# Kernel tuning notes

Measured on AMD Instinct MI355X. Metric: run time of the kernel, lower is better.

The kernel has to match this reference:

```python
import jax, jax.numpy as jnp
import numpy as np

N_NODES = 50000
EMB = 256
HEADS = 2
N_BASE_EDGES = 100000


def setup_inputs() -> dict:
    key = jax.random.key(0)
    ks = jax.random.split(key, 12)
    x = jax.random.normal(ks[0], (N_NODES, EMB), dtype=jnp.float32)
    # bipartite edges: sources in left half, targets in right half -> no self-loops
    src = jax.random.randint(ks[1], (N_BASE_EDGES,), 0, N_NODES // 2)
    dst = jax.random.randint(ks[2], (N_BASE_EDGES,), N_NODES // 2, N_NODES)
    edge_index = jnp.stack([src, dst]).astype(jnp.int64)
    hd = EMB // HEADS
    s = 0.02
    params = {
        "Wkqv": jax.random.normal(ks[3], (EMB, 3 * EMB), dtype=jnp.float32) * s,
        "bkqv": jnp.zeros((3 * EMB,), dtype=jnp.float32),
        "W1": jax.random.normal(ks[4], (2 * hd, hd), dtype=jnp.float32) * s,
        "b1": jnp.zeros((hd,), dtype=jnp.float32),
        "W2": jax.random.normal(ks[5], (hd, 1), dtype=jnp.float32) * s,
        "b2": jnp.zeros((1,), dtype=jnp.float32),
        "Wout": jax.random.normal(ks[6], (EMB, EMB), dtype=jnp.float32) * s,
        "bout": jnp.zeros((EMB,), dtype=jnp.float32),
    }
    return {"x": x, "edge_index": edge_index, **params}


def reference(x, edge_index, Wkqv, bkqv, W1, b1, W2, b2, Wout, bout):
    N, emb = x.shape
    H = HEADS
    hd = emb // H
    # MetaGNNNoEdgeAttr.forward preprocessing: make undirected + self loops.
    # Input is bipartite (no self-loops), so remove_self_loops is a no-op.
    ei = jnp.concatenate([edge_index, edge_index[::-1]], axis=1)
    loops = jnp.arange(N, dtype=edge_index.dtype)
    src = jnp.concatenate([ei[0], loops])  # j (message source)
    dst = jnp.concatenate([ei[1], loops])  # i (message target / softmax index)

    # single GNN layer (n_layers=1)
    kqv = x @ Wkqv + bkqv  # [N, 3*emb]
    q = kqv[dst, :emb].reshape(-1, H, hd)                                  # [E,H,hd]
    k = kqv[src, emb:2 * emb].reshape(-1, H, hd) / jnp.sqrt(jnp.float32(hd))
    v = kqv[src, 2 * emb:].reshape(-1, H, hd)

    h = jax.nn.relu(jnp.concatenate([k, q], axis=-1) @ W1 + b1)  # [E,H,hd]
    a = (h @ W2 + b2).squeeze(-1)                                # [E,H]

    # segment softmax over destination nodes (every node has a self-loop)
    m = jax.ops.segment_max(a, dst, num_segments=N)              # [N,H]
    ex = jnp.exp(a - m[dst])
    s = jax.ops.segment_sum(ex, dst, num_segments=N)             # [N,H]
    alpha = ex / (s[dst] + 1e-16)                                # [E,H]

    msg = (alpha[..., None] * v).reshape(-1, emb) @ Wout + bout  # [E,emb]
    out = jax.ops.segment_sum(msg, dst, num_segments=N)          # [N,emb]
    return jax.nn.relu(out) + x
```

## Files before the change

kernel.cpp:

```cpp
#include <hip/hip_runtime.h>
#include <hip/hip_bf16.h>

#define EMB 256

typedef __bf16 bf16_t;
typedef __attribute__((ext_vector_type(8))) __bf16 bf16x8;
typedef __attribute__((ext_vector_type(4))) __bf16 bf16x4;
typedef __attribute__((ext_vector_type(4))) float floatx4;

__device__ __forceinline__ int eidx(const int* __restrict__ p, int is64, long long k){
  return is64 ? p[2*k] : p[(int)k];
}
__device__ __forceinline__ void async_load16(const void* g, void* l){
  __builtin_amdgcn_global_load_lds(
      (const __attribute__((address_space(1))) unsigned int*)g,
      (__attribute__((address_space(3))) unsigned int*)l,
      16, 0, 0);
}
__device__ __forceinline__ float4 cvt4(bf16x4 v){
  return make_float4((float)v.x, (float)v.y, (float)v.z, (float)v.w);
}

__global__ void detect_kernel(const int* __restrict__ ei, int* __restrict__ flag){
  int z = (ei[1]==0) + (ei[3]==0) + (ei[5]==0) + (ei[7]==0);
  *flag = (z == 4) ? 1 : 0;
}

__global__ void cvt_x_kernel(const float* __restrict__ x, bf16_t* __restrict__ xb, int n4){
  int t = blockIdx.x*blockDim.x + threadIdx.x;
  if (t >= n4) return;
  const float4 v = *(const float4*)(x + (size_t)t*4);
  bf16x4 o = { (bf16_t)v.x, (bf16_t)v.y, (bf16_t)v.z, (bf16_t)v.w };
  *(bf16x4*)(xb + (size_t)t*4) = o;
}

__global__ void prep_weights(const float* __restrict__ Wkqv, const float* __restrict__ bkqv,
                             const float* __restrict__ W1,
                             bf16_t* __restrict__ WcombT, float* __restrict__ bcomb){
  int n = blockIdx.x * blockDim.x + threadIdx.x;
  int c = blockIdx.y;
  if (n >= 768) return;
  const float rs = rsqrtf(128.0f);
  bool isBias = (c == 256);
  const float* arow = isBias ? bkqv : (Wkqv + (size_t)c*768);
  float val;
  if (n < 256){
    int h = n >> 7, d = n & 127;
    float s = 0.f;
    for (int t = 0; t < 128; ++t)
      s = fmaf(arow[h*128 + t], W1[(size_t)(128 + t)*128 + d], s);
    val = s;
  } else {
    int r = n - 256;
    int h = r >> 8, t8 = r & 255;
    int g = t8 >> 3, half = (t8 >> 2) & 1, dd = t8 & 3;
    int d = g*4 + dd;
    if (half == 0){
      float s = 0.f;
      for (int t = 0; t < 128; ++t)
        s = fmaf(arow[256 + h*128 + t], W1[(size_t)t*128 + d], s);
      val = s * rs;
    } else {
      val = arow[512 + h*128 + d];
    }
  }
  if (isBias) bcomb[n] = val;
  else        WcombT[(size_t)n*256 + c] = (bf16_t)val;
}

__global__ void prep_wout(const float* __restrict__ W, bf16_t* __restrict__ Wt){
  int t = blockIdx.x*blockDim.x + threadIdx.x;
  int n = t & 255, c = t >> 8;
  Wt[(size_t)n*256 + c] = (bf16_t)W[(size_t)c*256 + n];
}

__global__ void deg_kernel(const int* __restrict__ ei, const int* __restrict__ flag,
                           int* __restrict__ deg, int E0, int Nn){
  int t = blockIdx.x*blockDim.x + threadIdx.x;
  if (t >= 2*E0) return;
  int is64 = *flag;
  int i = (t < E0) ? eidx(ei,is64,(long long)E0+t) : eidx(ei,is64,t-E0);
  i = min(max(i,0), Nn-1);
  atomicAdd(deg + i, 1);
}

__global__ __launch_bounds__(1024) void scan_kernel(const int* __restrict__ deg,
                                                    int* __restrict__ off, int N){
  __shared__ int wsum[16];
  __shared__ int carry_s;
  int tid = threadIdx.x, lane = tid & 63, w = tid >> 6;
  if (tid == 0) carry_s = 0;
  __syncthreads();
  for (int base = 0; base < N; base += 1024){
    int carry = carry_s;
    int v = (base + tid < N) ? (deg[base + tid] + 1) : 0;
    int incl = v;
    #pragma unroll
    for (int o = 1; o < 64; o <<= 1){
      int t = __shfl_up(incl, o, 64);
      if (lane >= o) incl += t;
    }
    if (lane == 63) wsum[w] = incl;
    __syncthreads();
    if (w == 0 && lane < 16){
      int sv = wsum[lane];
      #pragma unroll
      for (int o = 1; o < 16; o <<= 1){
        int t = __shfl_up(sv, o, 64);
        if (lane >= o) sv += t;
      }
      wsum[lane] = sv;
    }
    __syncthreads();
    int wpref = (w == 0) ? 0 : wsum[w-1];
    if (base + tid < N) off[base + tid] = carry + wpref + incl - v;
    __syncthreads();
    if (tid == 1023) carry_s = carry + wsum[15];
    __syncthreads();
  }
  if (threadIdx.x == 0) off[N] = carry_s;
}

__global__ void scatter_kernel(const int* __restrict__ ei, const int* __restrict__ flag,
                               const int* __restrict__ off, int* __restrict__ cursor,
                               int* __restrict__ bj, int E0, int Nn){
  int e = blockIdx.x*blockDim.x + threadIdx.x;
  int E = 2*E0 + Nn;
  if (e >= E) return;
  int is64 = *flag;
  int j, i;
  if (e < E0){ j = eidx(ei,is64,e); i = eidx(ei,is64,(long long)E0+e); }
  else if (e < 2*E0){ int t = e - E0; i = eidx(ei,is64,t); j = eidx(ei,is64,(long long)E0+t); }
  else { i = j = e - 2*E0; }
  i = min(max(i,0), Nn-1); j = min(max(j,0), Nn-1);
  int pos = atomicAdd(cursor + i, 1);
  bj[off[i] + pos] = j;
}

template<int MODE, typename OutT>
__global__ __launch_bounds__(256) void mfma_gemm(
    const bf16_t* __restrict__ A, const bf16_t* __restrict__ Bt,
    const float* __restrict__ bias, OutT* __restrict__ C,
    int M, int N,
    const int* __restrict__ deg, const float* __restrict__ xres)
{
  __shared__ bf16_t As[2][128*32];
  __shared__ bf16_t Bs[2][128*32];
  const int tid = threadIdx.x;
  const int wave = tid >> 6, lane = tid & 63;
  const int row16 = lane & 15, quad = lane >> 4;

  const int nn = N >> 7;
  const int bid = blockIdx.x;
  const int strip = bid / (8*nn);
  const int inner = bid % (8*nn);
  const int m0 = (strip*8 + (inner & 7)) * 128;
  const int n0 = (inner >> 3) * 128;
  const int wm = (wave >> 1) * 64, wn = (wave & 1) * 64;

  const int f0 = wave*2, f1 = wave*2 + 1;
  const int gm0 = min(m0 + f0*16 + row16, M-1);
  const int gm1 = min(m0 + f1*16 + row16, M-1);
  const int gn0 = n0 + f0*16 + row16;
  const int gn1 = n0 + f1*16 + row16;

  async_load16(A  + (size_t)gm0*256 + quad*8, (char*)As[0] + f0*1024);
  async_load16(A  + (size_t)gm1*256 + quad*8, (char*)As[0] + f1*1024);
  async_load16(Bt + (size_t)gn0*256 + quad*8, (char*)Bs[0] + f0*1024);
  async_load16(Bt + (size_t)gn1*256 + quad*8, (char*)Bs[0] + f1*1024);

  floatx4 acc[4][4];
  #pragma unroll
  for (int a=0;a<4;++a)
    #pragma unroll
    for (int b=0;b<4;++b) acc[a][b] = (floatx4){0.f,0.f,0.f,0.f};

  #pragma unroll
  for (int kt = 0; kt < 8; ++kt){
    const int cur = kt & 1, nxt = cur ^ 1;
    const int k1 = (kt+1)*32;

    __syncthreads();

    if (kt < 7){
      async_load16(A  + (size_t)gm0*256 + k1 + quad*8, (char*)As[nxt] + f0*1024);
      async_load16(A  + (size_t)gm1*256 + k1 + quad*8, (char*)As[nxt] + f1*1024);
      async_load16(Bt + (size_t)gn0*256 + k1 + quad*8, (char*)Bs[nxt] + f0*1024);
      async_load16(Bt + (size_t)gn1*256 + k1 + quad*8, (char*)Bs[nxt] + f1*1024);
    }

    bf16x8 af[4], bfr[4];
    #pragma unroll
    for (int t = 0; t < 4; ++t){
      af[t]  = *(const bf16x8*)((const char*)As[cur] + ((wm>>4)+t)*1024 + lane*16);
      bfr[t] = *(const bf16x8*)((const char*)Bs[cur] + ((wn>>4)+t)*1024 + lane*16);
    }
    #pragma unroll
    for (int mt=0;mt<4;++mt)
      #pragma unroll
      for (int nt=0;nt<4;++nt)
        acc[mt][nt] = __builtin_amdgcn_mfma_f32_16x16x32_bf16(af[mt], bfr[nt], acc[mt][nt], 0,0,0);
  }

  #pragma unroll
  for (int mt=0;mt<4;++mt){
    #pragma unroll
    for (int r=0;r<4;++r){
      int m = m0 + wm + mt*16 + quad*4 + r;
      if (m >= M) continue;
      float dg = (MODE==1) ? (float)(deg[m]+1) : 0.f;
      #pragma unroll
      for (int nt=0;nt<4;++nt){
        int n = n0 + wn + nt*16 + row16;
        float v = acc[mt][nt][r];
        if (MODE == 0){
          v += bias[n];
        } else {
          v = fmaxf(v + dg*bias[n], 0.f) + xres[(size_t)m*N + n];
        }
        C[(size_t)m*N + n] = (OutT)v;
      }
    }
  }
}

__global__ __launch_bounds__(256) void fused_attn_kernel(
    const bf16_t* __restrict__ P, const int* __restrict__ bj, const int* __restrict__ off,
    const float* __restrict__ b1, const float* __restrict__ W2, const float* __restrict__ b2,
    bf16_t* __restrict__ aggb, int Nn)
{
  int i = blockIdx.x * (blockDim.x >> 6) + (threadIdx.x >> 6);
  if (i >= Nn) return;
  int lane = threadIdx.x & 63;
  int h = lane >> 5, g = lane & 31, d = g * 4;

  const float4 qv  = cvt4(*(const bf16x4*)(P + (size_t)i*768 + h*128 + d));
  const float4 b1v = *(const float4*)(b1 + d);
  const float4 w2v = *(const float4*)(W2 + d);
  const float b2v  = b2[0];

  float m = -3.0e38f, s = 0.f;
  float4 acc = make_float4(0.f,0.f,0.f,0.f);
  int s0 = off[i], s1 = off[i+1];
  for (int t = s0; t < s1; ++t){
    int j = bj[t];
    bf16x8 kvv = *(const bf16x8*)(P + (size_t)j*768 + 256 + h*256 + g*8);
    float kx = (float)kvv[0], ky = (float)kvv[1], kz = (float)kvv[2], kw = (float)kvv[3];
    float vx = (float)kvv[4], vy = (float)kvv[5], vz = (float)kvv[6], vw = (float)kvv[7];
    float p = fmaxf(qv.x+kx+b1v.x, 0.f)*w2v.x
            + fmaxf(qv.y+ky+b1v.y, 0.f)*w2v.y
            + fmaxf(qv.z+kz+b1v.z, 0.f)*w2v.z
            + fmaxf(qv.w+kw+b1v.w, 0.f)*w2v.w;
    #pragma unroll
    for (int o = 16; o >= 1; o >>= 1)
      p += __shfl_xor(p, o, 64);
    float a = p + b2v;
    float mn = fmaxf(m, a);
    float sc = __expf(m - mn);
    float e  = __expf(a - mn);
    s = s*sc + e;
    acc.x = fmaf(acc.x, sc, e*vx);
    acc.y = fmaf(acc.y, sc, e*vy);
    acc.z = fmaf(acc.z, sc, e*vz);
    acc.w = fmaf(acc.w, sc, e*vw);
    m = mn;
  }
  float inv = 1.f / (s + 1e-16f);
  bf16x4 ob = { (bf16_t)(acc.x*inv), (bf16_t)(acc.y*inv), (bf16_t)(acc.z*inv), (bf16_t)(acc.w*inv) };
  *(bf16x4*)(aggb + (size_t)i*256 + h*128 + d) = ob;
}

extern "C" void kernel_launch(void* const* d_in, const int* in_sizes, int n_in,
                              void* d_out, int out_size, void* d_ws, size_t ws_size,
                              hipStream_t stream)
{
  const float* x     = (const float*)d_in[0];
  const int*   ei    = (const int*)d_in[1];
  const float* Wkqv  = (const float*)d_in[2];
  const float* bkqv  = (const float*)d_in[3];
  const float* W1    = (const float*)d_in[4];
  const float* b1    = (const float*)d_in[5];
  const float* W2    = (const float*)d_in[6];
  const float* b2    = (const float*)d_in[7];
  const float* Wout  = (const float*)d_in[8];
  const float* bout  = (const float*)d_in[9];
  float* out = (float*)d_out;

  const int N  = in_sizes[0] / EMB;
  const int E0 = in_sizes[1] / 2;
  const int E  = 2*E0 + N;

  float* base = (float*)d_ws;
  bf16_t* WcombT = (bf16_t*)base;
  float*  bcomb  = base + 98304;
  bf16_t* WoutT  = (bf16_t*)(base + 98304 + 768);
  bf16_t* xb     = (bf16_t*)(base + 131840);
  bf16_t* Pb     = (bf16_t*)(base + 131840 + 6400000);
  bf16_t* aggb   = (bf16_t*)(Pb + (size_t)N*768);
  int* deg       = (int*)(aggb + (size_t)N*256);
  int* cursor    = deg + N;
  int* flag      = cursor + N;
  int* off       = flag + 1;
  int* bj        = off + (N+1);

  hipMemsetAsync(deg, 0, (size_t)2*N*sizeof(int), stream);

  detect_kernel<<<1,1,0,stream>>>(ei, flag);
  cvt_x_kernel<<<((N*EMB/4)+255)/256,256,0,stream>>>(x, xb, N*EMB/4);
  prep_weights<<<dim3(3,257),256,0,stream>>>(Wkqv, bkqv, W1, WcombT, bcomb);
  prep_wout<<<256,256,0,stream>>>(Wout, WoutT);

  deg_kernel<<<(2*E0+255)/256,256,0,stream>>>(ei, flag, deg, E0, N);
  scan_kernel<<<1,1024,0,stream>>>(deg, off, N);
  scatter_kernel<<<(E+255)/256,256,0,stream>>>(ei, flag, off, cursor, bj, E0, N);

  const int nm8 = (((N+127)/128) + 7) & ~7;
  mfma_gemm<0, bf16_t><<<nm8*6,256,0,stream>>>(xb, WcombT, bcomb, Pb, N, 768, nullptr, nullptr);
  fused_attn_kernel<<<(N+3)/4,256,0,stream>>>(Pb, bj, off, b1, W2, b2, aggb, N);
  mfma_gemm<1, float><<<nm8*2,256,0,stream>>>(aggb, WoutT, bout, out, N, 256, deg, x);
}
```

Baseline: 333.7 us.

## Load GEMM fragments directly from global memory, dropping LDS staging

Removes the LDS double-buffered async global-to-LDS staging in the MFMA GEMM. Each wave now loads its A and B fragments straight from global memory into registers, with no barriers. A launch-bounds occupancy hint of 4 blocks per unit is added. This removes the shared memory footprint and the per-k-step synchronisation. In exchange, tiles shared between waves are no longer reused, so each element is fetched twice from global/L2, and there is no explicit prefetch to hide load latency.

```diff
diff --git a/kernel.cpp b/kernel.cpp
--- a/kernel.cpp
+++ b/kernel.cpp
@@ -10,12 +10,6 @@
 
 __device__ __forceinline__ int eidx(const int* __restrict__ p, int is64, long long k){
   return is64 ? p[2*k] : p[(int)k];
-}
-__device__ __forceinline__ void async_load16(const void* g, void* l){
-  __builtin_amdgcn_global_load_lds(
-      (const __attribute__((address_space(1))) unsigned int*)g,
-      (__attribute__((address_space(3))) unsigned int*)l,
-      16, 0, 0);
 }
 __device__ __forceinline__ float4 cvt4(bf16x4 v){
   return make_float4((float)v.x, (float)v.y, (float)v.z, (float)v.w);
@@ -138,14 +132,12 @@
 }
 
 template<int MODE, typename OutT>
-__global__ __launch_bounds__(256) void mfma_gemm(
+__global__ __launch_bounds__(256, 4) void mfma_gemm(
     const bf16_t* __restrict__ A, const bf16_t* __restrict__ Bt,
     const float* __restrict__ bias, OutT* __restrict__ C,
     int M, int N,
     const int* __restrict__ deg, const float* __restrict__ xres)
 {
-  __shared__ bf16_t As[2][128*32];
-  __shared__ bf16_t Bs[2][128*32];
   const int tid = threadIdx.x;
   const int wave = tid >> 6, lane = tid & 63;
   const int row16 = lane & 15, quad = lane >> 4;
@@ -158,16 +150,14 @@
   const int n0 = (inner >> 3) * 128;
   const int wm = (wave >> 1) * 64, wn = (wave & 1) * 64;
 
-  const int f0 = wave*2, f1 = wave*2 + 1;
-  const int gm0 = min(m0 + f0*16 + row16, M-1);
-  const int gm1 = min(m0 + f1*16 + row16, M-1);
-  const int gn0 = n0 + f0*16 + row16;
-  const int gn1 = n0 + f1*16 + row16;
-
-  async_load16(A  + (size_t)gm0*256 + quad*8, (char*)As[0] + f0*1024);
-  async_load16(A  + (size_t)gm1*256 + quad*8, (char*)As[0] + f1*1024);
-  async_load16(Bt + (size_t)gn0*256 + quad*8, (char*)Bs[0] + f0*1024);
-  async_load16(Bt + (size_t)gn1*256 + quad*8, (char*)Bs[0] + f1*1024);
+  const bf16_t* Ap[4];
+  const bf16_t* Bp[4];
+  #pragma unroll
+  for (int t = 0; t < 4; ++t){
+    int rm = min(m0 + wm + t*16 + row16, M-1);
+    Ap[t] = A  + (size_t)rm*256 + quad*8;
+    Bp[t] = Bt + (size_t)(n0 + wn + t*16 + row16)*256 + quad*8;
+  }
 
   floatx4 acc[4][4];
   #pragma unroll
@@ -177,23 +167,11 @@
 
   #pragma unroll
   for (int kt = 0; kt < 8; ++kt){
-    const int cur = kt & 1, nxt = cur ^ 1;
-    const int k1 = (kt+1)*32;
-
-    __syncthreads();
-
-    if (kt < 7){
-      async_load16(A  + (size_t)gm0*256 + k1 + quad*8, (char*)As[nxt] + f0*1024);
-      async_load16(A  + (size_t)gm1*256 + k1 + quad*8, (char*)As[nxt] + f1*1024);
-      async_load16(Bt + (size_t)gn0*256 + k1 + quad*8, (char*)Bs[nxt] + f0*1024);
-      async_load16(Bt + (size_t)gn1*256 + k1 + quad*8, (char*)Bs[nxt] + f1*1024);
-    }
-
     bf16x8 af[4], bfr[4];
     #pragma unroll
     for (int t = 0; t < 4; ++t){
-      af[t]  = *(const bf16x8*)((const char*)As[cur] + ((wm>>4)+t)*1024 + lane*16);
-      bfr[t] = *(const bf16x8*)((const char*)Bs[cur] + ((wn>>4)+t)*1024 + lane*16);
+      af[t]  = *(const bf16x8*)(Ap[t] + kt*32);
+      bfr[t] = *(const bf16x8*)(Bp[t] + kt*32);
     }
     #pragma unroll
     for (int mt=0;mt<4;++mt)
```

After: 380.0 us. 13.9% more time.

## Triple-buffer GEMM LDS tiles with explicit vmcnt waits and MFMA priority

Applied to the files above, without the earlier changes.

Replaces the double-buffered k-loop in the MFMA GEMM with a three-stage LDS ring, issuing async global->LDS loads two tiles ahead. Each phase waits with a hand-set vmcnt count instead of a full drain, so only the current tile's loads must have landed. MFMA issue priority is raised with s_setprio around the compute block. This uses half again as much shared memory, which can lower occupancy, and depends on exact vmcnt accounting being correct.

```diff
diff --git a/kernel.cpp b/kernel.cpp
--- a/kernel.cpp
+++ b/kernel.cpp
@@ -144,8 +144,8 @@
     int M, int N,
     const int* __restrict__ deg, const float* __restrict__ xres)
 {
-  __shared__ bf16_t As[2][128*32];
-  __shared__ bf16_t Bs[2][128*32];
+  __shared__ bf16_t As[3][128*32];
+  __shared__ bf16_t Bs[3][128*32];
   const int tid = threadIdx.x;
   const int wave = tid >> 6, lane = tid & 63;
   const int row16 = lane & 15, quad = lane >> 4;
@@ -164,10 +164,10 @@
   const int gn0 = n0 + f0*16 + row16;
   const int gn1 = n0 + f1*16 + row16;
 
-  async_load16(A  + (size_t)gm0*256 + quad*8, (char*)As[0] + f0*1024);
-  async_load16(A  + (size_t)gm1*256 + quad*8, (char*)As[0] + f1*1024);
-  async_load16(Bt + (size_t)gn0*256 + quad*8, (char*)Bs[0] + f0*1024);
-  async_load16(Bt + (size_t)gn1*256 + quad*8, (char*)Bs[0] + f1*1024);
+  const size_t aoff0 = (size_t)gm0*256 + quad*8;
+  const size_t aoff1 = (size_t)gm1*256 + quad*8;
+  const size_t boff0 = (size_t)gn0*256 + quad*8;
+  const size_t boff1 = (size_t)gn1*256 + quad*8;
 
   floatx4 acc[4][4];
   #pragma unroll
@@ -175,32 +175,43 @@
     #pragma unroll
     for (int b=0;b<4;++b) acc[a][b] = (floatx4){0.f,0.f,0.f,0.f};
 
-  #pragma unroll
-  for (int kt = 0; kt < 8; ++kt){
-    const int cur = kt & 1, nxt = cur ^ 1;
-    const int k1 = (kt+1)*32;
-
-    __syncthreads();
-
-    if (kt < 7){
-      async_load16(A  + (size_t)gm0*256 + k1 + quad*8, (char*)As[nxt] + f0*1024);
-      async_load16(A  + (size_t)gm1*256 + k1 + quad*8, (char*)As[nxt] + f1*1024);
-      async_load16(Bt + (size_t)gn0*256 + k1 + quad*8, (char*)Bs[nxt] + f0*1024);
-      async_load16(Bt + (size_t)gn1*256 + k1 + quad*8, (char*)Bs[nxt] + f1*1024);
-    }
-
-    bf16x8 af[4], bfr[4];
-    #pragma unroll
-    for (int t = 0; t < 4; ++t){
-      af[t]  = *(const bf16x8*)((const char*)As[cur] + ((wm>>4)+t)*1024 + lane*16);
-      bfr[t] = *(const bf16x8*)((const char*)Bs[cur] + ((wn>>4)+t)*1024 + lane*16);
-    }
-    #pragma unroll
-    for (int mt=0;mt<4;++mt)
-      #pragma unroll
-      for (int nt=0;nt<4;++nt)
-        acc[mt][nt] = __builtin_amdgcn_mfma_f32_16x16x32_bf16(af[mt], bfr[nt], acc[mt][nt], 0,0,0);
-  }
+  #define STAGE(kt, buf) do{ \
+    async_load16(A  + aoff0 + (kt)*32, (char*)As[buf] + f0*1024); \
+    async_load16(A  + aoff1 + (kt)*32, (char*)As[buf] + f1*1024); \
+    async_load16(Bt + boff0 + (kt)*32, (char*)Bs[buf] + f0*1024); \
+    async_load16(Bt + boff1 + (kt)*32, (char*)Bs[buf] + f1*1024); }while(0)
+
+  STAGE(0,0); STAGE(1,1);
+
+  #define PHASE(kt, vm) do{ \
+    if ((kt)+2 < 8) STAGE((kt)+2, ((kt)+2)%3); \
+    asm volatile("s_waitcnt vmcnt(" #vm ")" ::: "memory"); \
+    __builtin_amdgcn_s_barrier(); \
+    __builtin_amdgcn_sched_barrier(0); \
+    bf16x8 af[4], bfr[4]; \
+    _Pragma("unroll") \
+    for (int t = 0; t < 4; ++t){ \
+      af[t]  = *(const bf16x8*)((const char*)As[(kt)%3] + ((wm>>4)+t)*1024 + lane*16); \
+      bfr[t] = *(const bf16x8*)((const char*)Bs[(kt)%3] + ((wn>>4)+t)*1024 + lane*16); \
+    } \
+    __builtin_amdgcn_s_setprio(1); \
+    _Pragma("unroll") \
+    for (int mt=0;mt<4;++mt) \
+      _Pragma("unroll") \
+      for (int nt=0;nt<4;++nt) \
+        acc[mt][nt] = __builtin_amdgcn_mfma_f32_16x16x32_bf16(af[mt], bfr[nt], acc[mt][nt], 0,0,0); \
+    __builtin_amdgcn_s_setprio(0); \
+    if ((kt) < 7){ \
+      asm volatile("s_waitcnt lgkmcnt(0)" ::: "memory"); \
+      __builtin_amdgcn_sched_barrier(0); \
+      __builtin_amdgcn_s_barrier(); \
+    } }while(0)
+
+  PHASE(0,8); PHASE(1,8); PHASE(2,8); PHASE(3,8);
+  PHASE(4,8); PHASE(5,8); PHASE(6,4); PHASE(7,0);
+
+  #undef PHASE
+  #undef STAGE
 
   #pragma unroll
   for (int mt=0;mt<4;++mt){
```

Measured after the change: 343.7 us. +3.0%, slower.
